# Performance work log

Hardware: AMD Instinct MI355X
Metric: run time of the kernel (lower is better)

## Reference

```python
import jax, jax.numpy as jnp
import numpy as np

B, N, DIM = 4, 2048, 1024
HEADS, DIM_HEAD = 16, 64
INNER = HEADS * DIM_HEAD


def setup_inputs() -> dict:
    key = jax.random.key(0)
    kx, kw = jax.random.split(key)
    x = jax.random.normal(kx, (B, N, DIM), dtype=jnp.float32)
    # Dense kernel [in_features, out_features], no bias
    w_qkv = jax.random.normal(kw, (DIM, 3 * INNER), dtype=jnp.float32) * (DIM ** -0.5)
    return {"x": x, "w_qkv": w_qkv}


def reference(x, w_qkv):
    scale = DIM_HEAD ** (-0.5)
    qkv = jnp.einsum('bnc,cf->bnf', x, w_qkv)  # [B, N, 3*INNER]
    q, k, v = jnp.split(qkv, 3, axis=-1)
    # 'b n (h d) -> b h n d'
    def to_heads(t):
        return t.reshape(B, N, HEADS, DIM_HEAD).transpose(0, 2, 1, 3)
    q, k, v = map(to_heads, (q, k, v))
    dots = jnp.einsum('bhid,bhjd->bhij', q, k) * scale  # [B, H, N, N]
    attn = jax.nn.softmax(dots, axis=-1)
    out = jnp.einsum('bhij,bhjd->bhid', attn, v)  # [B, H, N, D]
    # 'b h n d -> b n (h d)'
    return out.transpose(0, 2, 1, 3).reshape(B, N, INNER)
```

## Files before the change

### kernel.cpp

```cpp
#include <hip/hip_runtime.h>
#include <hip/hip_bf16.h>
#include <math.h>

typedef __bf16 bf16x4 __attribute__((ext_vector_type(4)));
typedef __bf16 bf16x8 __attribute__((ext_vector_type(8)));
typedef float f32x4 __attribute__((ext_vector_type(4)));

#define MFMA16(a, b, c) __builtin_amdgcn_mfma_f32_16x16x32_bf16(a, b, c, 0, 0, 0)

__global__ __launch_bounds__(256) void convert_x(const float* __restrict__ in,
                                                 __bf16* __restrict__ out) {
  int i = blockIdx.x * 256 + threadIdx.x;
  float4 v = ((const float4*)in)[i];
  bf16x4 o = {(__bf16)v.x, (__bf16)v.y, (__bf16)v.z, (__bf16)v.w};
  *(bf16x4*)&out[i * 4] = o;
}

__global__ __launch_bounds__(256) void transpose_w(const float* __restrict__ W,
                                                   __bf16* __restrict__ Wt) {
  __shared__ __bf16 tile[64][65];
  const int bx = blockIdx.x;
  const int by = blockIdx.y;
  const int t = threadIdx.x;
  const int lr = t >> 6;
  const int lc = t & 63;
#pragma unroll
  for (int i = 0; i < 16; ++i) {
    int r = lr + i * 4;
    tile[r][lc] = (__bf16)W[(size_t)(by * 64 + r) * 3072 + bx * 64 + lc];
  }
  __syncthreads();
#pragma unroll
  for (int i = 0; i < 16; ++i) {
    int r = lr + i * 4;
    Wt[(size_t)(bx * 64 + r) * 1024 + by * 64 + lc] = tile[lc][r];
  }
}

#define TM 128
#define TN 128
#define BK 32
#define LDA 48

__global__ __launch_bounds__(256) void gemm_qkv(const __bf16* __restrict__ X,
                                                const __bf16* __restrict__ Wt,
                                                __bf16* __restrict__ QKV) {
  __shared__ __bf16 As[TM * LDA];
  __shared__ __bf16 Bs[TN * LDA];
  const int n0 = blockIdx.x * TN;
  const int m0 = blockIdx.y * TM;
  const int t = threadIdx.x;
  const int lane = t & 63;
  const int wave = t >> 6;
  const int quad = lane >> 4;
  const int l16 = lane & 15;
  const int wm = (wave & 1) * 64;
  const int wn = (wave >> 1) * 64;
  const int sr = t >> 2;
  const int sk = (t & 3) * 8;

  f32x4 acc[4][4] = {};

  for (int k0 = 0; k0 < 1024; k0 += BK) {
    bf16x8 a0 = *(const bf16x8*)&X[(size_t)(m0 + sr) * 1024 + k0 + sk];
    bf16x8 a1 = *(const bf16x8*)&X[(size_t)(m0 + sr + 64) * 1024 + k0 + sk];
    bf16x8 b0 = *(const bf16x8*)&Wt[(size_t)(n0 + sr) * 1024 + k0 + sk];
    bf16x8 b1 = *(const bf16x8*)&Wt[(size_t)(n0 + sr + 64) * 1024 + k0 + sk];
    __syncthreads();
    *(bf16x8*)&As[sr * LDA + sk] = a0;
    *(bf16x8*)&As[(sr + 64) * LDA + sk] = a1;
    *(bf16x8*)&Bs[sr * LDA + sk] = b0;
    *(bf16x8*)&Bs[(sr + 64) * LDA + sk] = b1;
    __syncthreads();

    bf16x8 af[4], bf[4];
#pragma unroll
    for (int mi = 0; mi < 4; ++mi)
      af[mi] = *(const bf16x8*)&As[(wm + mi * 16 + l16) * LDA + quad * 8];
#pragma unroll
    for (int ni = 0; ni < 4; ++ni)
      bf[ni] = *(const bf16x8*)&Bs[(wn + ni * 16 + l16) * LDA + quad * 8];
#pragma unroll
    for (int mi = 0; mi < 4; ++mi)
#pragma unroll
      for (int ni = 0; ni < 4; ++ni)
        acc[mi][ni] = MFMA16(af[mi], bf[ni], acc[mi][ni]);
  }

#pragma unroll
  for (int mi = 0; mi < 4; ++mi)
#pragma unroll
    for (int ni = 0; ni < 4; ++ni)
#pragma unroll
      for (int r = 0; r < 4; ++r) {
        int row = m0 + wm + mi * 16 + quad * 4 + r;
        int col = n0 + wn + ni * 16 + l16;
        QKV[(size_t)row * 3072 + col] = (__bf16)acc[mi][ni][r];
      }
}

__global__ __launch_bounds__(256) void transpose_v(const __bf16* __restrict__ QKV,
                                                   __bf16* __restrict__ Vt) {
  __shared__ __bf16 tile[64][65];
  const int k0 = blockIdx.x * 64;
  const int h = blockIdx.y;
  const int b = blockIdx.z;
  const int t = threadIdx.x;
  const int lr = t >> 6;
  const int lc = t & 63;
  const __bf16* src = QKV + (size_t)b * 2048 * 3072 + 2048 + h * 64;
  __bf16* dst = Vt + (size_t)(b * 16 + h) * 64 * 2048;
#pragma unroll
  for (int i = 0; i < 16; ++i) {
    int r = lr + i * 4;
    tile[r][lc] = src[(size_t)(k0 + r) * 3072 + lc];
  }
  __syncthreads();
#pragma unroll
  for (int i = 0; i < 16; ++i) {
    int d = lr + i * 4;
    dst[(size_t)d * 2048 + k0 + lc] = tile[lc][d];
  }
}

#define AT_LD 72

__global__ __launch_bounds__(256) void attn(const __bf16* __restrict__ QKV,
                                            const __bf16* __restrict__ Vt,
                                            float* __restrict__ Out) {
  const int h = blockIdx.y;
  const int b = blockIdx.z;
  const int t = threadIdx.x;
  const int lane = t & 63;
  const int wave = t >> 6;
  const int quad = lane >> 4;
  const int l16 = lane & 15;
  const int q0w = blockIdx.x * 128 + wave * 32;

  const size_t base = (size_t)b * 2048 * 3072;
  const __bf16* Qb = QKV + base + h * 64;
  const __bf16* Kb = QKV + base + 1024 + h * 64;
  const __bf16* Vtb = Vt + (size_t)(b * 16 + h) * 64 * 2048;

  __shared__ __bf16 Ks[64 * AT_LD];
  __shared__ __bf16 Vs[64 * AT_LD];
  __shared__ __bf16 Ps[4][32 * AT_LD];
  __bf16* Psw = Ps[wave];

  bf16x8 qf[2][2];
#pragma unroll
  for (int mi = 0; mi < 2; ++mi)
#pragma unroll
    for (int kc = 0; kc < 2; ++kc)
      qf[mi][kc] = *(const bf16x8*)&Qb[(size_t)(q0w + mi * 16 + l16) * 3072 + kc * 32 + quad * 8];

  f32x4 o[2][4] = {};
  float lsum[2] = {0.0f, 0.0f};

  const int srow = t >> 2;
  const int sc = (t & 3) * 16;

  for (int kv0 = 0; kv0 < 2048; kv0 += 64) {
    bf16x8 k0v = *(const bf16x8*)&Kb[(size_t)(kv0 + srow) * 3072 + sc];
    bf16x8 k1v = *(const bf16x8*)&Kb[(size_t)(kv0 + srow) * 3072 + sc + 8];
    bf16x8 v0v = *(const bf16x8*)&Vtb[(size_t)srow * 2048 + kv0 + sc];
    bf16x8 v1v = *(const bf16x8*)&Vtb[(size_t)srow * 2048 + kv0 + sc + 8];
    __syncthreads();
    *(bf16x8*)&Ks[srow * AT_LD + sc] = k0v;
    *(bf16x8*)&Ks[srow * AT_LD + sc + 8] = k1v;
    *(bf16x8*)&Vs[srow * AT_LD + sc] = v0v;
    *(bf16x8*)&Vs[srow * AT_LD + sc + 8] = v1v;
    __syncthreads();

    f32x4 st[2][4];
#pragma unroll
    for (int mt = 0; mt < 4; ++mt) {
      bf16x8 kf0 = *(const bf16x8*)&Ks[(mt * 16 + l16) * AT_LD + quad * 8];
      bf16x8 kf1 = *(const bf16x8*)&Ks[(mt * 16 + l16) * AT_LD + 32 + quad * 8];
#pragma unroll
      for (int mi = 0; mi < 2; ++mi) {
        f32x4 z = {};
        z = MFMA16(kf0, qf[mi][0], z);
        z = MFMA16(kf1, qf[mi][1], z);
        st[mi][mt] = z;
      }
    }

#pragma unroll
    for (int mi = 0; mi < 2; ++mi)
#pragma unroll
      for (int mt = 0; mt < 4; ++mt) {
        bf16x4 pk;
#pragma unroll
        for (int r = 0; r < 4; ++r) {
          float p = __expf(st[mi][mt][r] * 0.125f);
          lsum[mi] += p;
          pk[r] = (__bf16)p;
        }
        *(bf16x4*)&Psw[(mi * 16 + l16) * AT_LD + mt * 16 + quad * 4] = pk;
      }

    bf16x8 pf[2][2];
#pragma unroll
    for (int mi = 0; mi < 2; ++mi)
#pragma unroll
      for (int kc = 0; kc < 2; ++kc)
        pf[mi][kc] = *(const bf16x8*)&Psw[(mi * 16 + l16) * AT_LD + kc * 32 + quad * 8];

#pragma unroll
    for (int dt = 0; dt < 4; ++dt) {
      bf16x8 vf0 = *(const bf16x8*)&Vs[(dt * 16 + l16) * AT_LD + quad * 8];
      bf16x8 vf1 = *(const bf16x8*)&Vs[(dt * 16 + l16) * AT_LD + 32 + quad * 8];
#pragma unroll
      for (int mi = 0; mi < 2; ++mi) {
        o[mi][dt] = MFMA16(pf[mi][0], vf0, o[mi][dt]);
        o[mi][dt] = MFMA16(pf[mi][1], vf1, o[mi][dt]);
      }
    }
  }

#pragma unroll
  for (int mi = 0; mi < 2; ++mi) {
    lsum[mi] += __shfl_xor(lsum[mi], 16);
    lsum[mi] += __shfl_xor(lsum[mi], 32);
  }

#pragma unroll
  for (int mi = 0; mi < 2; ++mi)
#pragma unroll
    for (int r = 0; r < 4; ++r) {
      float inv = 1.0f / __shfl(lsum[mi], quad * 4 + r);
      int orow = b * 2048 + q0w + mi * 16 + quad * 4 + r;
#pragma unroll
      for (int dt = 0; dt < 4; ++dt)
        Out[(size_t)orow * 1024 + h * 64 + dt * 16 + l16] = o[mi][dt][r] * inv;
    }
}

extern "C" void kernel_launch(void* const* d_in, const int* in_sizes, int n_in,
                              void* d_out, int out_size, void* d_ws, size_t ws_size,
                              hipStream_t stream) {
  const float* x = (const float*)d_in[0];
  const float* w = (const float*)d_in[1];
  float* out = (float*)d_out;

  __bf16* Wt = (__bf16*)d_ws;
  __bf16* QKV = Wt + (size_t)3072 * 1024;
  __bf16* Xb = QKV + (size_t)8192 * 3072;
  __bf16* Vtr = Xb;

  convert_x<<<8192, 256, 0, stream>>>(x, Xb);
  transpose_w<<<dim3(48, 16), 256, 0, stream>>>(w, Wt);
  gemm_qkv<<<dim3(24, 64), 256, 0, stream>>>(Xb, Wt, QKV);
  transpose_v<<<dim3(32, 16, 4), 256, 0, stream>>>(QKV, Vtr);
  attn<<<dim3(16, 16, 4), 256, 0, stream>>>(QKV, Vtr, out);
}
```

Measured before the change: 262.8 us.

## Fold softmax scale into W, use direct-to-LDS loads, widen attention query tile

The softmax scale times log2(e) is folded into the Q columns of the weight during the transpose, so attention can call the raw exp2 instruction without a multiply. The QKV GEMM now fetches tiles straight into shared memory with global_load_lds and an unpadded layout, removing the register staging. Each attention wave now handles 64 query rows instead of 32, which halves the grid and reuses each K/V tile across twice as many queries. The trade-offs are more registers per thread, fewer blocks in flight, and possible LDS bank conflicts in the unpadded GEMM layout.

```diff
diff --git a/kernel.cpp b/kernel.cpp
--- a/kernel.cpp
+++ b/kernel.cpp
@@ -7,6 +7,13 @@
 typedef float f32x4 __attribute__((ext_vector_type(4)));
 
 #define MFMA16(a, b, c) __builtin_amdgcn_mfma_f32_16x16x32_bf16(a, b, c, 0, 0, 0)
+#define QSCALE 0.1803368801111204f
+
+__device__ __forceinline__ void gload_lds16(const __bf16* g, __bf16* l) {
+  __builtin_amdgcn_global_load_lds((const __attribute__((address_space(1))) void*)g,
+                                   (__attribute__((address_space(3))) void*)l,
+                                   16, 0, 0);
+}
 
 __global__ __launch_bounds__(256) void convert_x(const float* __restrict__ in,
                                                  __bf16* __restrict__ out) {
@@ -24,10 +31,11 @@
   const int t = threadIdx.x;
   const int lr = t >> 6;
   const int lc = t & 63;
+  const float sc = (bx < 16) ? QSCALE : 1.0f;
 #pragma unroll
   for (int i = 0; i < 16; ++i) {
     int r = lr + i * 4;
-    tile[r][lc] = (__bf16)W[(size_t)(by * 64 + r) * 3072 + bx * 64 + lc];
+    tile[r][lc] = (__bf16)(W[(size_t)(by * 64 + r) * 3072 + bx * 64 + lc] * sc);
   }
   __syncthreads();
 #pragma unroll
@@ -36,55 +44,51 @@
     Wt[(size_t)(bx * 64 + r) * 1024 + by * 64 + lc] = tile[lc][r];
   }
 }
-
-#define TM 128
-#define TN 128
-#define BK 32
-#define LDA 48
 
 __global__ __launch_bounds__(256) void gemm_qkv(const __bf16* __restrict__ X,
                                                 const __bf16* __restrict__ Wt,
                                                 __bf16* __restrict__ QKV) {
-  __shared__ __bf16 As[TM * LDA];
-  __shared__ __bf16 Bs[TN * LDA];
-  const int n0 = blockIdx.x * TN;
-  const int m0 = blockIdx.y * TM;
+  __shared__ __bf16 As[128 * 32];
+  __shared__ __bf16 Bs[128 * 32];
   const int t = threadIdx.x;
   const int lane = t & 63;
   const int wave = t >> 6;
   const int quad = lane >> 4;
   const int l16 = lane & 15;
+  const int n0 = blockIdx.x * 128;
+  const int m0 = blockIdx.y * 128;
   const int wm = (wave & 1) * 64;
   const int wn = (wave >> 1) * 64;
-  const int sr = t >> 2;
-  const int sk = (t & 3) * 8;
+
+  const __bf16* Ag = &X[(size_t)(m0 + wave * 16 + (lane >> 2)) * 1024 + (lane & 3) * 8];
+  const __bf16* Bg = &Wt[(size_t)(n0 + wave * 16 + (lane >> 2)) * 1024 + (lane & 3) * 8];
+  __bf16* As0 = &As[wave * 512];
+  __bf16* As1 = &As[2048 + wave * 512];
+  __bf16* Bs0 = &Bs[wave * 512];
+  __bf16* Bs1 = &Bs[2048 + wave * 512];
 
   f32x4 acc[4][4] = {};
 
-  for (int k0 = 0; k0 < 1024; k0 += BK) {
-    bf16x8 a0 = *(const bf16x8*)&X[(size_t)(m0 + sr) * 1024 + k0 + sk];
-    bf16x8 a1 = *(const bf16x8*)&X[(size_t)(m0 + sr + 64) * 1024 + k0 + sk];
-    bf16x8 b0 = *(const bf16x8*)&Wt[(size_t)(n0 + sr) * 1024 + k0 + sk];
-    bf16x8 b1 = *(const bf16x8*)&Wt[(size_t)(n0 + sr + 64) * 1024 + k0 + sk];
-    __syncthreads();
-    *(bf16x8*)&As[sr * LDA + sk] = a0;
-    *(bf16x8*)&As[(sr + 64) * LDA + sk] = a1;
-    *(bf16x8*)&Bs[sr * LDA + sk] = b0;
-    *(bf16x8*)&Bs[(sr + 64) * LDA + sk] = b1;
+  for (int k0 = 0; k0 < 1024; k0 += 32) {
+    gload_lds16(Ag + k0, As0);
+    gload_lds16(Ag + (size_t)64 * 1024 + k0, As1);
+    gload_lds16(Bg + k0, Bs0);
+    gload_lds16(Bg + (size_t)64 * 1024 + k0, Bs1);
     __syncthreads();
 
     bf16x8 af[4], bf[4];
 #pragma unroll
     for (int mi = 0; mi < 4; ++mi)
-      af[mi] = *(const bf16x8*)&As[(wm + mi * 16 + l16) * LDA + quad * 8];
+      af[mi] = *(const bf16x8*)&As[(wm + mi * 16 + l16) * 32 + quad * 8];
 #pragma unroll
     for (int ni = 0; ni < 4; ++ni)
-      bf[ni] = *(const bf16x8*)&Bs[(wn + ni * 16 + l16) * LDA + quad * 8];
+      bf[ni] = *(const bf16x8*)&Bs[(wn + ni * 16 + l16) * 32 + quad * 8];
 #pragma unroll
     for (int mi = 0; mi < 4; ++mi)
 #pragma unroll
       for (int ni = 0; ni < 4; ++ni)
         acc[mi][ni] = MFMA16(af[mi], bf[ni], acc[mi][ni]);
+    __syncthreads();
   }
 
 #pragma unroll
@@ -135,7 +139,7 @@
   const int wave = t >> 6;
   const int quad = lane >> 4;
   const int l16 = lane & 15;
-  const int q0w = blockIdx.x * 128 + wave * 32;
+  const int q0w = blockIdx.x * 256 + wave * 64;
 
   const size_t base = (size_t)b * 2048 * 3072;
   const __bf16* Qb = QKV + base + h * 64;
@@ -144,18 +148,18 @@
 
   __shared__ __bf16 Ks[64 * AT_LD];
   __shared__ __bf16 Vs[64 * AT_LD];
-  __shared__ __bf16 Ps[4][32 * AT_LD];
+  __shared__ __bf16 Ps[4][64 * AT_LD];
   __bf16* Psw = Ps[wave];
 
-  bf16x8 qf[2][2];
-#pragma unroll
-  for (int mi = 0; mi < 2; ++mi)
+  bf16x8 qf[4][2];
+#pragma unroll
+  for (int mi = 0; mi < 4; ++mi)
 #pragma unroll
     for (int kc = 0; kc < 2; ++kc)
       qf[mi][kc] = *(const bf16x8*)&Qb[(size_t)(q0w + mi * 16 + l16) * 3072 + kc * 32 + quad * 8];
 
-  f32x4 o[2][4] = {};
-  float lsum[2] = {0.0f, 0.0f};
+  f32x4 o[4][4] = {};
+  float lsum[4] = {0.0f, 0.0f, 0.0f, 0.0f};
 
   const int srow = t >> 2;
   const int sc = (t & 3) * 16;
@@ -172,37 +176,34 @@
     *(bf16x8*)&Vs[srow * AT_LD + sc + 8] = v1v;
     __syncthreads();
 
-    f32x4 st[2][4];
 #pragma unroll
     for (int mt = 0; mt < 4; ++mt) {
       bf16x8 kf0 = *(const bf16x8*)&Ks[(mt * 16 + l16) * AT_LD + quad * 8];
       bf16x8 kf1 = *(const bf16x8*)&Ks[(mt * 16 + l16) * AT_LD + 32 + quad * 8];
-#pragma unroll
-      for (int mi = 0; mi < 2; ++mi) {
+      f32x4 stt[4];
+#pragma unroll
+      for (int mi = 0; mi < 4; ++mi) {
         f32x4 z = {};
         z = MFMA16(kf0, qf[mi][0], z);
         z = MFMA16(kf1, qf[mi][1], z);
-        st[mi][mt] = z;
-      }
-    }
-
-#pragma unroll
-    for (int mi = 0; mi < 2; ++mi)
-#pragma unroll
-      for (int mt = 0; mt < 4; ++mt) {
+        stt[mi] = z;
+      }
+#pragma unroll
+      for (int mi = 0; mi < 4; ++mi) {
         bf16x4 pk;
 #pragma unroll
         for (int r = 0; r < 4; ++r) {
-          float p = __expf(st[mi][mt][r] * 0.125f);
+          float p = __builtin_amdgcn_exp2f(stt[mi][r]);
           lsum[mi] += p;
           pk[r] = (__bf16)p;
         }
         *(bf16x4*)&Psw[(mi * 16 + l16) * AT_LD + mt * 16 + quad * 4] = pk;
       }
-
-    bf16x8 pf[2][2];
-#pragma unroll
-    for (int mi = 0; mi < 2; ++mi)
+    }
+
+    bf16x8 pf[4][2];
+#pragma unroll
+    for (int mi = 0; mi < 4; ++mi)
 #pragma unroll
       for (int kc = 0; kc < 2; ++kc)
         pf[mi][kc] = *(const bf16x8*)&Psw[(mi * 16 + l16) * AT_LD + kc * 32 + quad * 8];
@@ -212,7 +213,7 @@
       bf16x8 vf0 = *(const bf16x8*)&Vs[(dt * 16 + l16) * AT_LD + quad * 8];
       bf16x8 vf1 = *(const bf16x8*)&Vs[(dt * 16 + l16) * AT_LD + 32 + quad * 8];
 #pragma unroll
-      for (int mi = 0; mi < 2; ++mi) {
+      for (int mi = 0; mi < 4; ++mi) {
         o[mi][dt] = MFMA16(pf[mi][0], vf0, o[mi][dt]);
         o[mi][dt] = MFMA16(pf[mi][1], vf1, o[mi][dt]);
       }
@@ -220,13 +221,13 @@
   }
 
 #pragma unroll
-  for (int mi = 0; mi < 2; ++mi) {
+  for (int mi = 0; mi < 4; ++mi) {
     lsum[mi] += __shfl_xor(lsum[mi], 16);
     lsum[mi] += __shfl_xor(lsum[mi], 32);
   }
 
 #pragma unroll
-  for (int mi = 0; mi < 2; ++mi)
+  for (int mi = 0; mi < 4; ++mi)
 #pragma unroll
     for (int r = 0; r < 4; ++r) {
       float inv = 1.0f / __shfl(lsum[mi], quad * 4 + r);
@@ -253,5 +254,5 @@
   transpose_w<<<dim3(48, 16), 256, 0, stream>>>(w, Wt);
   gemm_qkv<<<dim3(24, 64), 256, 0, stream>>>(Xb, Wt, QKV);
   transpose_v<<<dim3(32, 16, 4), 256, 0, stream>>>(QKV, Vtr);
-  attn<<<dim3(16, 16, 4), 256, 0, stream>>>(QKV, Vtr, out);
-}
+  attn<<<dim3(8, 16, 4), 256, 0, stream>>>(QKV, Vtr, out);
+}
```

Result: slower. 287.1 us (+9.3%).
